# Performance work log

Measured on AMD Instinct MI355X. Metric: run time of the kernel, lower is better.

## Reference

```python
import jax, jax.numpy as jnp
import numpy as np
from jax import lax

BITS_W = 8   # bitwidth_weight
BITS_A = 16  # bitwidth_act
N_KEEP = 32


def fake_quantize(w, bits, rounded=True):
    # Power-of-two scale fake quantization (min-max observer -> quanta).
    maxabs = jnp.max(jnp.abs(w))
    quanta = jnp.ceil(jnp.log2(maxabs + 1e-12)) - (bits - 1)
    scale = jnp.exp2(quanta)
    q = w / scale
    if rounded:
        q = jnp.round(q)
    lo = float(-(2 ** (bits - 1)))
    hi = float(2 ** (bits - 1) - 1)
    q = jnp.clip(q, lo, hi)
    return q * scale


def ste(w, fq):
    # straight-through estimator: forward = fq, gradient = identity
    return w + lax.stop_gradient(fq - w)


def setup_inputs() -> dict:
    key = jax.random.key(0)
    k1, k2, k3 = jax.random.split(key, 3)
    B, C, T = 16, 64, 8192
    O = 256
    x = jax.random.normal(k1, (B, C, T), dtype=jnp.float32)
    # kaiming-uniform-like init scale for a linear with fan_in = C*N_KEEP
    fan_in = C * N_KEEP
    weight = jax.random.normal(k2, (O, fan_in), dtype=jnp.float32) / np.sqrt(fan_in)
    bias = jax.random.normal(k3, (O,), dtype=jnp.float32) / np.sqrt(fan_in)
    return {"x": x, "weight": weight, "bias": bias, "n_discard": 8}


def reference(x, weight, bias, n_discard):
    # x: [B, C, T] channels-first stream; weight: [O, C*n_keep]
    B, C, T = x.shape
    O, CK = weight.shape
    K = CK // C  # n_keep
    # fake-quantize weights (rounded) and bias, with STE
    qw = ste(weight, fake_quantize(weight, BITS_W, rounded=True))
    qb = ste(bias, fake_quantize(bias, BITS_A, rounded=True))
    # windowed flat linear == causal conv with extra delay of n_discard:
    # out[t] contracts x[:, :, t-n_discard-K+1 : t-n_discard+1] (zero-padded) with qw
    xp = jnp.pad(x, ((0, 0), (0, 0), (K - 1 + n_discard, 0)))
    w3 = qw.reshape(O, C, K)  # [O, C, K] matching (C, K) row-major flatten of the window
    y = lax.conv_general_dilated(
        xp, w3, window_strides=(1,), padding='VALID',
        dimension_numbers=('NCH', 'OIH', 'NCH'))  # [B, O, T + n_discard]
    y = y[..., :T] + qb[None, :, None]
    # output requantization (activation fake-quant, round=False in F block)
    y = ste(y, fake_quantize(y, BITS_A, rounded=False))
    return y
```

## Files before the change

kernel.cpp:

```cpp
#include <hip/hip_runtime.h>
#include <hip/hip_bf16.h>

typedef __bf16 bf16x8 __attribute__((ext_vector_type(8)));
typedef float f32x4 __attribute__((ext_vector_type(4)));

#define T_LEN 8192
#define C_IN 64
#define O_OUT 256
#define KW 32
#define CKTOT 2048
#define UPAD 8256
#define ROWB 128

#define WFRAG_OFF 256
#define XTB_OFF (WFRAG_OFF + O_OUT*CKTOT*2)

#define BM 64
#define BT 256
#define TILE_ROWS 288

__global__ void k_maxabs(const float* __restrict__ w, unsigned int* __restrict__ out, int n) {
  float m = 0.f;
  for (int i = blockIdx.x * blockDim.x + threadIdx.x; i < n; i += gridDim.x * blockDim.x)
    m = fmaxf(m, fabsf(w[i]));
  #pragma unroll
  for (int off = 32; off; off >>= 1)
    m = fmaxf(m, __shfl_down(m, off, 64));
  if ((threadIdx.x & 63) == 0) atomicMax(out, __float_as_uint(m));
}

__global__ void k_quantw(const float* __restrict__ w, const unsigned int* __restrict__ mab,
                         unsigned short* __restrict__ wfrag) {
  int idx = blockIdx.x * blockDim.x + threadIdx.x;
  if (idx >= O_OUT * CKTOT) return;
  float maxabs = __uint_as_float(*mab);
  float quanta = ceilf(log2f(maxabs + 1e-12f)) - 7.0f;
  float scale = exp2f(quanta), inv = exp2f(-quanta);
  float q = rintf(w[idx] * inv);
  q = fminf(fmaxf(q, -128.f), 127.f);
  __hip_bfloat16 hv = __float2bfloat16(q * scale);
  int o = idx >> 11, ck = idx & 2047;
  int c = ck >> 5, k = ck & 31;
  int om = o >> 4, r = o & 15;
  int h = c >> 5, ci = c & 31, g = ci >> 3, j = ci & 7;
  int off = ((((om * 2 + h) * 32 + k) * 64) + (r + 16 * g)) * 8 + j;
  wfrag[off] = *(unsigned short*)&hv;
}

__global__ void k_xT(const float* __restrict__ x, const int* __restrict__ ndp,
                     unsigned short* __restrict__ xT) {
  __shared__ float tile[64][65];
  const int P = 31 + *ndp;
  const int b = blockIdx.y;
  const int u0 = blockIdx.x * 64;
  const int lane = threadIdx.x & 63, rw = threadIdx.x >> 6;
  const float* xb = x + (size_t)b * C_IN * T_LEN;
  const int t = u0 - P + lane;
  const bool tin = (t >= 0) && (t < T_LEN);
  #pragma unroll
  for (int it = 0; it < 16; ++it) {
    int c = it * 4 + rw;
    tile[c][lane] = tin ? xb[(size_t)c * T_LEN + t] : 0.f;
  }
  __syncthreads();
  unsigned short* xo = xT + ((size_t)b * UPAD + u0) * C_IN;
  #pragma unroll
  for (int it = 0; it < 16; ++it) {
    int i = it * 4 + rw;
    __hip_bfloat16 hv = __float2bfloat16(tile[lane][i]);
    xo[(size_t)i * C_IN + lane] = *(unsigned short*)&hv;
  }
}

__global__ __launch_bounds__(256, 2)
void k_main(const unsigned short* __restrict__ xT,
            const int4* __restrict__ wf,
            const float* __restrict__ bias,
            float* __restrict__ out) {
  __shared__ int4 lds4[TILE_ROWS * ROWB / 16];
  unsigned char* lds = (unsigned char*)lds4;
  const int tid = threadIdx.x;
  const int lane = tid & 63;
  const int w = tid >> 6;
  const int lr = lane & 15, g = lane >> 4;
  const int tb = blockIdx.x * BT;
  const int ob = blockIdx.y * BM;
  const int b = blockIdx.z;

  const unsigned char* src = (const unsigned char*)(xT + ((size_t)b * UPAD + tb) * C_IN);
  #pragma unroll
  for (int it = 0; it < TILE_ROWS * ROWB / (256 * 16); ++it) {
    int a = (it * 256 + tid) * 16;
    int d = a ^ (((a >> 7) & 7) << 4);
    *(int4*)(lds + d) = *(const int4*)(src + a);
  }
  __syncthreads();

  f32x4 acc[4][4];
  #pragma unroll
  for (int m = 0; m < 4; ++m)
    #pragma unroll
    for (int n = 0; n < 4; ++n)
      acc[m][n] = (f32x4){0.f, 0.f, 0.f, 0.f};

  const int om0 = ob >> 4;
  const int lt0 = w * 64;

  for (int h = 0; h < 2; ++h) {
    for (int k = 0; k < KW; ++k) {
      bf16x8 afr[4];
      #pragma unroll
      for (int m = 0; m < 4; ++m)
        afr[m] = __builtin_bit_cast(bf16x8, wf[(((om0 + m) * 2 + h) * 32 + k) * 64 + lane]);
      #pragma unroll
      for (int n = 0; n < 4; ++n) {
        int row = lt0 + n * 16 + k + lr;
        int ad = (row * ROWB + h * 64 + g * 16) ^ ((row & 7) << 4);
        bf16x8 bfr = __builtin_bit_cast(bf16x8, *(const int4*)(lds + ad));
        #pragma unroll
        for (int m = 0; m < 4; ++m)
          acc[m][n] = __builtin_amdgcn_mfma_f32_16x16x32_bf16(afr[m], bfr, acc[m][n], 0, 0, 0);
      }
    }
  }

  float* obp = out + (size_t)b * O_OUT * T_LEN;
  #pragma unroll
  for (int m = 0; m < 4; ++m) {
    #pragma unroll
    for (int r = 0; r < 4; ++r) {
      int o = ob + m * 16 + g * 4 + r;
      float bv = bias[o];
      float* orow = obp + (size_t)o * T_LEN + tb + lt0 + lr;
      #pragma unroll
      for (int n = 0; n < 4; ++n)
        orow[n * 16] = acc[m][n][r] + bv;
    }
  }
}

extern "C" void kernel_launch(void* const* d_in, const int* in_sizes, int n_in,
                              void* d_out, int out_size, void* d_ws, size_t ws_size,
                              hipStream_t stream) {
  const float* x    = (const float*)d_in[0];
  const float* wt   = (const float*)d_in[1];
  const float* bias = (const float*)d_in[2];
  const int*   ndp  = (const int*)d_in[3];
  float* out = (float*)d_out;
  unsigned char* ws = (unsigned char*)d_ws;
  unsigned int*   mab   = (unsigned int*)ws;
  unsigned short* wfrag = (unsigned short*)(ws + WFRAG_OFF);
  unsigned short* xTb   = (unsigned short*)(ws + XTB_OFF);
  const int B = in_sizes[0] / (C_IN * T_LEN);

  hipMemsetAsync(mab, 0, 4, stream);
  k_maxabs<<<256, 256, 0, stream>>>(wt, mab, O_OUT * CKTOT);
  k_quantw<<<(O_OUT * CKTOT + 255) / 256, 256, 0, stream>>>(wt, mab, wfrag);
  k_xT<<<dim3(UPAD / 64, B), 256, 0, stream>>>(x, ndp, xTb);
  k_main<<<dim3(T_LEN / BT, O_OUT / BM, B), 256, 0, stream>>>(xTb, (const int4*)wfrag, bias, out);
}
```

Measured before the change: 276.8 us.

## Vectorize prep-kernel stores, double-buffer weight fragments, swap MFMA operands for vector output stores

The quantize and transpose kernels now pack eight bf16 values per thread and write them with 16-byte stores instead of scattered 2-byte stores. In the main kernel the MFMA operands are swapped so that x is the A operand and the weights are B. That puts four consecutive time steps in each lane's accumulator, so results go out as float4 stores. Weight fragments are loaded one k-step ahead (double-buffered) to overlap global loads with MFMA, and launch bounds ask for 4 blocks per SM. The added register pressure from the extra buffers under a tighter occupancy target could cause spills.

```diff
diff --git a/kernel.cpp b/kernel.cpp
--- a/kernel.cpp
+++ b/kernel.cpp
@@ -30,21 +30,27 @@
 }
 
 __global__ void k_quantw(const float* __restrict__ w, const unsigned int* __restrict__ mab,
-                         unsigned short* __restrict__ wfrag) {
-  int idx = blockIdx.x * blockDim.x + threadIdx.x;
-  if (idx >= O_OUT * CKTOT) return;
+                         int4* __restrict__ wfrag) {
+  int tid = blockIdx.x * blockDim.x + threadIdx.x;
+  if (tid >= O_OUT * CKTOT / 8) return;
   float maxabs = __uint_as_float(*mab);
   float quanta = ceilf(log2f(maxabs + 1e-12f)) - 7.0f;
   float scale = exp2f(quanta), inv = exp2f(-quanta);
-  float q = rintf(w[idx] * inv);
-  q = fminf(fmaxf(q, -128.f), 127.f);
-  __hip_bfloat16 hv = __float2bfloat16(q * scale);
-  int o = idx >> 11, ck = idx & 2047;
-  int c = ck >> 5, k = ck & 31;
-  int om = o >> 4, r = o & 15;
-  int h = c >> 5, ci = c & 31, g = ci >> 3, j = ci & 7;
-  int off = ((((om * 2 + h) * 32 + k) * 64) + (r + 16 * g)) * 8 + j;
-  wfrag[off] = *(unsigned short*)&hv;
+  int L = tid & 63;
+  int r = L & 15, g = L >> 4;
+  int rest = tid >> 6;
+  int k = rest & 31, h = (rest >> 5) & 1, om = rest >> 6;
+  int o = om * 16 + r;
+  unsigned short res[8];
+  #pragma unroll
+  for (int j = 0; j < 8; ++j) {
+    int c = h * 32 + g * 8 + j;
+    float q = rintf(w[o * CKTOT + c * 32 + k] * inv);
+    q = fminf(fmaxf(q, -128.f), 127.f);
+    __hip_bfloat16 hv = __float2bfloat16(q * scale);
+    res[j] = *(unsigned short*)&hv;
+  }
+  wfrag[tid] = *(int4*)res;
 }
 
 __global__ void k_xT(const float* __restrict__ x, const int* __restrict__ ndp,
@@ -65,14 +71,20 @@
   __syncthreads();
   unsigned short* xo = xT + ((size_t)b * UPAD + u0) * C_IN;
   #pragma unroll
-  for (int it = 0; it < 16; ++it) {
-    int i = it * 4 + rw;
-    __hip_bfloat16 hv = __float2bfloat16(tile[lane][i]);
-    xo[(size_t)i * C_IN + lane] = *(unsigned short*)&hv;
+  for (int p = 0; p < 2; ++p) {
+    int u = p * 32 + (threadIdx.x >> 3);
+    int jg = threadIdx.x & 7;
+    unsigned short res[8];
+    #pragma unroll
+    for (int i = 0; i < 8; ++i) {
+      __hip_bfloat16 hv = __float2bfloat16(tile[jg * 8 + i][u]);
+      res[i] = *(unsigned short*)&hv;
+    }
+    *(int4*)(xo + (size_t)u * C_IN + jg * 8) = *(int4*)res;
   }
 }
 
-__global__ __launch_bounds__(256, 2)
+__global__ __launch_bounds__(256, 4)
 void k_main(const unsigned short* __restrict__ xT,
             const int4* __restrict__ wf,
             const float* __restrict__ bias,
@@ -106,35 +118,47 @@
   const int om0 = ob >> 4;
   const int lt0 = w * 64;
 
-  for (int h = 0; h < 2; ++h) {
-    for (int k = 0; k < KW; ++k) {
-      bf16x8 afr[4];
-      #pragma unroll
-      for (int m = 0; m < 4; ++m)
-        afr[m] = __builtin_bit_cast(bf16x8, wf[(((om0 + m) * 2 + h) * 32 + k) * 64 + lane]);
-      #pragma unroll
-      for (int n = 0; n < 4; ++n) {
-        int row = lt0 + n * 16 + k + lr;
-        int ad = (row * ROWB + h * 64 + g * 16) ^ ((row & 7) << 4);
-        bf16x8 bfr = __builtin_bit_cast(bf16x8, *(const int4*)(lds + ad));
-        #pragma unroll
-        for (int m = 0; m < 4; ++m)
-          acc[m][n] = __builtin_amdgcn_mfma_f32_16x16x32_bf16(afr[m], bfr, acc[m][n], 0, 0, 0);
-      }
-    }
+  #define LDW(dst, kk) { int h_ = (kk) >> 5, k_ = (kk) & 31;                              \
+    _Pragma("unroll")                                                                     \
+    for (int n = 0; n < 4; ++n)                                                           \
+      dst[n] = __builtin_bit_cast(bf16x8, wf[(((om0 + n) * 2 + h_) * 32 + k_) * 64 + lane]); }
+  #define LDA(dst, kk) { int h_ = (kk) >> 5, k_ = (kk) & 31;                              \
+    _Pragma("unroll")                                                                     \
+    for (int m = 0; m < 4; ++m) {                                                         \
+      int row_ = lt0 + m * 16 + k_ + lr;                                                  \
+      int ad_ = (row_ * ROWB + h_ * 64 + g * 16) ^ ((row_ & 7) << 4);                     \
+      dst[m] = __builtin_bit_cast(bf16x8, *(const int4*)(lds + ad_)); } }
+  #define MM(xf, wfr)                                                                     \
+    _Pragma("unroll")                                                                     \
+    for (int n = 0; n < 4; ++n)                                                           \
+      _Pragma("unroll")                                                                   \
+      for (int m = 0; m < 4; ++m)                                                         \
+        acc[m][n] = __builtin_amdgcn_mfma_f32_16x16x32_bf16(xf[m], wfr[n], acc[m][n], 0, 0, 0);
+
+  bf16x8 wA[4], wB[4], xf[4];
+  LDW(wA, 0);
+  for (int kk = 0; kk < 64; kk += 2) {
+    LDW(wB, kk + 1);
+    LDA(xf, kk);
+    MM(xf, wA);
+    if (kk + 2 < 64) LDW(wA, kk + 2);
+    LDA(xf, kk + 1);
+    MM(xf, wB);
   }
 
+  float bv[4];
+  #pragma unroll
+  for (int n = 0; n < 4; ++n) bv[n] = bias[ob + n * 16 + lr];
   float* obp = out + (size_t)b * O_OUT * T_LEN;
   #pragma unroll
-  for (int m = 0; m < 4; ++m) {
+  for (int n = 0; n < 4; ++n) {
+    int o = ob + n * 16 + lr;
     #pragma unroll
-    for (int r = 0; r < 4; ++r) {
-      int o = ob + m * 16 + g * 4 + r;
-      float bv = bias[o];
-      float* orow = obp + (size_t)o * T_LEN + tb + lt0 + lr;
-      #pragma unroll
-      for (int n = 0; n < 4; ++n)
-        orow[n * 16] = acc[m][n][r] + bv;
+    for (int m = 0; m < 4; ++m) {
+      int t0 = tb + lt0 + m * 16 + g * 4;
+      f32x4 v = acc[m][n];
+      v[0] += bv[n]; v[1] += bv[n]; v[2] += bv[n]; v[3] += bv[n];
+      *(f32x4*)(obp + (size_t)o * T_LEN + t0) = v;
     }
   }
 }
@@ -155,7 +179,7 @@
 
   hipMemsetAsync(mab, 0, 4, stream);
   k_maxabs<<<256, 256, 0, stream>>>(wt, mab, O_OUT * CKTOT);
-  k_quantw<<<(O_OUT * CKTOT + 255) / 256, 256, 0, stream>>>(wt, mab, wfrag);
+  k_quantw<<<(O_OUT * CKTOT / 8 + 255) / 256, 256, 0, stream>>>(wt, mab, (int4*)wfrag);
   k_xT<<<dim3(UPAD / 64, B), 256, 0, stream>>>(x, ndp, xTb);
   k_main<<<dim3(T_LEN / BT, O_OUT / BM, B), 256, 0, stream>>>(xTb, (const int4*)wfrag, bias, out);
 }
```

Measured after the change: 285.3 us. 1.03x slower.
